# Performance work log

Hardware: AMD Instinct MI355X
Metric: run time of the kernel (lower is better)

The kernel has to match this reference:

```python
import jax, jax.numpy as jnp
import numpy as np

N, E, L, H, D_HID, D_IN, D_NEI, S_NEI, N_CLS = 30000, 480000, 2, 4, 128, 128, 64, 10, 2
HD = D_HID // H  # 32 per-head dim


def _mha(x, in_w, in_b, out_w, out_b, n_heads=4):
    # x: [N, S, D]; in_w: [D, 3D]; out_w: [D, D]
    n, s, d = x.shape
    hd = d // n_heads
    qkv = x @ in_w + in_b  # [N, S, 3D]
    q, k, v = jnp.split(qkv, 3, axis=-1)
    rs = lambda t: t.reshape(n, s, n_heads, hd).transpose(0, 2, 1, 3)  # [N,H,S,hd]
    q, k, v = rs(q), rs(k), rs(v)
    attn = jax.nn.softmax(jnp.einsum('nhqd,nhkd->nhqk', q, k) / np.sqrt(hd).astype(np.float32), axis=-1)
    o = jnp.einsum('nhqk,nhkd->nhqd', attn, v).transpose(0, 2, 1, 3).reshape(n, s, d)
    return o @ out_w + out_b


def _layer_norm(x, g, b, eps=1e-5):
    m = jnp.mean(x, axis=-1, keepdims=True)
    v = jnp.var(x, axis=-1, keepdims=True)
    return (x - m) * jax.lax.rsqrt(v + eps) * g + b


def _transformer_conv(src, dst, h, wq_i, bq_i, wk_i, bk_i, wv_i, bv_i):
    # per-head graph transformer conv: q from dst, k/v from src, edge softmax over dst
    q = (h @ wq_i + bq_i).reshape(N, H, HD)
    k = (h @ wk_i + bk_i).reshape(N, H, HD)
    v = (h @ wv_i + bv_i).reshape(N, H, HD)
    score = jnp.sum(q[dst] * k[src], axis=-1) / np.sqrt(HD).astype(np.float32)  # [E, H]
    smax = jax.ops.segment_max(score, dst, num_segments=N)  # [N, H]
    ex = jnp.exp(score - smax[dst])  # [E, H]
    denom = jax.ops.segment_sum(ex, dst, num_segments=N)  # [N, H]
    num = jax.ops.segment_sum(ex[:, :, None] * v[src], dst, num_segments=N)  # [N, H, HD]
    out = num / jnp.maximum(denom, 1e-9)[:, :, None]
    return out.reshape(N, D_HID)


def setup_inputs() -> dict:
    key = jax.random.key(0)
    ks = jax.random.split(key, 24)
    d = {}
    d['x'] = jax.random.normal(ks[0], (N, D_IN), jnp.float32)
    d['nei_features'] = jax.random.normal(ks[1], (N, S_NEI, D_NEI), jnp.float32)
    d['edge_index'] = jax.random.randint(ks[2], (L, 2, E), 0, N, jnp.int32)
    sc = 0.05
    d['w_in'] = jax.random.normal(ks[3], (D_IN, D_HID), jnp.float32) * sc
    d['b_in'] = jax.random.normal(ks[4], (D_HID,), jnp.float32) * sc
    d['mha_in_w'] = jax.random.normal(ks[5], (D_NEI, 3 * D_NEI), jnp.float32) * sc
    d['mha_in_b'] = jax.random.normal(ks[6], (3 * D_NEI,), jnp.float32) * sc
    d['mha_out_w'] = jax.random.normal(ks[7], (D_NEI, D_NEI), jnp.float32) * sc
    d['mha_out_b'] = jax.random.normal(ks[8], (D_NEI,), jnp.float32) * sc
    d['w_nei'] = jax.random.normal(ks[9], (D_NEI, D_HID), jnp.float32) * sc
    d['b_nei'] = jax.random.normal(ks[10], (D_HID,), jnp.float32) * sc
    d['wq'] = jax.random.normal(ks[11], (L, D_HID, D_HID), jnp.float32) * sc
    d['bq'] = jax.random.normal(ks[12], (L, D_HID), jnp.float32) * sc
    d['wk'] = jax.random.normal(ks[13], (L, D_HID, D_HID), jnp.float32) * sc
    d['bk'] = jax.random.normal(ks[14], (L, D_HID), jnp.float32) * sc
    d['wv'] = jax.random.normal(ks[15], (L, D_HID, D_HID), jnp.float32) * sc
    d['bv'] = jax.random.normal(ks[16], (L, D_HID), jnp.float32) * sc
    d['ln_g'] = jnp.ones((L, D_HID), jnp.float32)
    d['ln_b'] = jnp.zeros((L, D_HID), jnp.float32)
    d['w_out'] = jax.random.normal(ks[17], (D_HID, N_CLS), jnp.float32) * sc
    d['b_out'] = jnp.zeros((N_CLS,), jnp.float32)
    return d


def reference(x, nei_features, edge_index, w_in, b_in, mha_in_w, mha_in_b,
              mha_out_w, mha_out_b, w_nei, b_nei, wq, bq, wk, bk, wv, bv,
              ln_g, ln_b, w_out, b_out):
    h = x @ w_in + b_in  # input_proj
    # neighbor-feature self-attention branch (nn.MultiheadAttention, eval mode)
    nei = _mha(nei_features, mha_in_w, mha_in_b, mha_out_w, mha_out_b).mean(axis=1)
    h = h + (nei @ w_nei + b_nei)
    for i in range(L):
        src, dst = edge_index[i, 0], edge_index[i, 1]
        h = _transformer_conv(src, dst, h, wq[i], bq[i], wk[i], bk[i], wv[i], bv[i])
        h = jax.nn.relu(h)
        h = _layer_norm(h, ln_g[i], ln_b[i])
        # dropout is identity in eval mode
    return h @ w_out + b_out
```

## Files before the change

kernel.cpp:

```cpp
#include <hip/hip_runtime.h>
#include <hip/hip_bf16.h>

#define NN 30000
#define EE 480000

typedef __attribute__((ext_vector_type(8))) short short8;
typedef __attribute__((ext_vector_type(4))) short short4v;
typedef __attribute__((ext_vector_type(4))) float floatx4;
typedef unsigned short u16;

__device__ __forceinline__ u16 f2bf(float f) {
  union { float f; unsigned u; } v; v.f = f;
  unsigned u = v.u;
  u += 0x7FFFu + ((u >> 16) & 1u);
  return (u16)(u >> 16);
}
__device__ __forceinline__ float bf2f(u16 u) {
  union { unsigned u; float f; } v; v.u = ((unsigned)u) << 16;
  return v.f;
}
__device__ __forceinline__ float bflo(unsigned u) {
  union { unsigned x; float f; } v; v.x = u << 16; return v.f;
}
__device__ __forceinline__ float bfhi(unsigned u) {
  union { unsigned x; float f; } v; v.x = u & 0xFFFF0000u; return v.f;
}
__device__ __forceinline__ unsigned packbf(float a, float b) {
  return (unsigned)f2bf(a) | ((unsigned)f2bf(b) << 16);
}
__device__ __forceinline__ short8 pack8(float4 A, float4 B) {
  union { unsigned u[4]; short8 s; } r;
  r.u[0] = packbf(A.x, A.y);
  r.u[1] = packbf(A.z, A.w);
  r.u[2] = packbf(B.x, B.y);
  r.u[3] = packbf(B.z, B.w);
  return r.s;
}

#define MFMA32 __builtin_amdgcn_mfma_f32_16x16x32_bf16

#if __has_builtin(__builtin_amdgcn_mfma_f32_16x16x16bf16_1k)
__device__ __forceinline__ floatx4 MFMA16(short4v a, short4v b, floatx4 c) {
  return __builtin_amdgcn_mfma_f32_16x16x16bf16_1k(a, b, c, 0, 0, 0);
}
#else
__device__ __forceinline__ floatx4 MFMA16(short4v a, short4v b, floatx4 c) {
  asm volatile("v_mfma_f32_16x16x16_bf16 %0, %1, %2, %0"
               : "+v"(c) : "v"(a), "v"(b));
  return c;
}
#endif

__global__ __launch_bounds__(128) void k_fuse(
    const float* __restrict__ out_w, const float* __restrict__ out_b,
    const float* __restrict__ w_nei, const float* __restrict__ b_nei,
    const float* __restrict__ b_in,
    float* __restrict__ fusedW, float* __restrict__ fusedB) {
  int i = blockIdx.x, j = threadIdx.x;
  if (i < 64) {
    float a = 0.f;
    for (int kk = 0; kk < 64; ++kk) a = fmaf(out_w[i * 64 + kk], w_nei[kk * 128 + j], a);
    fusedW[i * 128 + j] = a;
  } else {
    float a = b_in[j] + b_nei[j];
    for (int kk = 0; kk < 64; ++kk) a = fmaf(out_b[kk], w_nei[kk * 128 + j], a);
    fusedB[j] = a;
  }
}

__global__ __launch_bounds__(128) void k_fuseB(
    const float* __restrict__ fusedW, const float* __restrict__ fusedB,
    const float* __restrict__ in_b, float* __restrict__ fusedB2) {
  int c = threadIdx.x;
  float a = fusedB[c];
  for (int d = 0; d < 64; ++d) a = fmaf(in_b[128 + d], fusedW[d * 128 + c], a);
  fusedB2[c] = a;
}

__global__ __launch_bounds__(128) void k_prepG(
    const float* __restrict__ in_w, const float* __restrict__ fusedW,
    float* __restrict__ G) {
  int row = blockIdx.x, c = threadIdx.x;
  int h = row >> 6, d = row & 63;
  float a = 0.f;
  for (int dd = 0; dd < 16; ++dd)
    a = fmaf(in_w[d * 192 + 128 + h * 16 + dd], fusedW[(h * 16 + dd) * 128 + c], a);
  G[row * 128 + c] = a;
}

__global__ __launch_bounds__(384) void k_prepP2(
    const float* __restrict__ w_in, const float* __restrict__ G,
    u16* __restrict__ wtP2) {
  int c = blockIdx.x, k = threadIdx.x;
  float v = (k < 128) ? w_in[(size_t)k * 128 + c] : G[(size_t)(k - 128) * 128 + c];
  wtP2[(size_t)c * 384 + k] = f2bf(v);
}

__global__ __launch_bounds__(64) void k_prepQK(
    const float* __restrict__ in_w, u16* __restrict__ wtQK) {
  int c = blockIdx.x, kk = threadIdx.x;
  float s = (c < 64) ? 0.25f : 1.f;
  wtQK[(size_t)c * 64 + kk] = f2bf(s * in_w[(size_t)kk * 192 + c]);
}

__global__ __launch_bounds__(128) void k_prepW(
    const float* __restrict__ wq, const float* __restrict__ wk,
    const float* __restrict__ wv, u16* __restrict__ wt3) {
  int bx = blockIdx.x;
  int l = bx / 384, rem = bx % 384, o = rem >> 7, c = rem & 127, k = threadIdx.x;
  const float* w = (o == 0 ? wq : (o == 1 ? wk : wv)) + (size_t)l * 16384;
  wt3[(size_t)bx * 128 + k] = f2bf(w[(size_t)k * 128 + c]);
}

__global__ __launch_bounds__(256) void k_prepX(const float* __restrict__ x, u16* __restrict__ xb) {
  int i = blockIdx.x * 256 + threadIdx.x;
  if (i < NN * 128 / 4) {
    float4 v = ((const float4*)x)[i];
    uint2 o;
    o.x = packbf(v.x, v.y);
    o.y = packbf(v.z, v.w);
    ((uint2*)xb)[i] = o;
  }
}

__global__ __launch_bounds__(640) void k_mha5(
    const float* __restrict__ xn,
    const u16* __restrict__ wtQK,
    const float* __restrict__ in_b,
    u16* __restrict__ Yb) {
  __shared__ unsigned qks[112 * 66];
  int t = threadIdx.x, w = t >> 6, l = t & 63;
  int lr = l & 15, lq = l >> 4;
  const floatx4 zf = {0.f, 0.f, 0.f, 0.f};
  size_t r0 = (size_t)blockIdx.x * 100;

  if (w < 7) {
    size_t arow = r0 + w * 16 + lr;
    if (arow > 299999) arow = 299999;
    const float* xp = xn + arow * 64 + lq * 8;
    float4 f0 = *(const float4*)xp;
    float4 f1 = *(const float4*)(xp + 4);
    float4 f2 = *(const float4*)(xp + 32);
    float4 f3 = *(const float4*)(xp + 36);
    short8 a0 = pack8(f0, f1), a1 = pack8(f2, f3);
    floatx4 acc[8];
#pragma unroll
    for (int ct = 0; ct < 8; ++ct) acc[ct] = zf;
#pragma unroll
    for (int ct = 0; ct < 8; ++ct) {
      const short8* bp = (const short8*)(wtQK + (size_t)(ct * 16 + lr) * 64);
      acc[ct] = MFMA32(a0, bp[lq], acc[ct], 0, 0, 0);
      acc[ct] = MFMA32(a1, bp[4 + lq], acc[ct], 0, 0, 0);
    }
#pragma unroll
    for (int ct = 0; ct < 4; ++ct) {
      float bq_ = in_b[ct * 16 + lr] * 0.25f;
      float bk_ = in_b[64 + ct * 16 + lr];
#pragma unroll
      for (int r = 0; r < 4; ++r)
        qks[(w * 16 + lq * 4 + r) * 66 + ct * 16 + lr] =
            packbf(acc[ct][r] + bq_, acc[ct + 4][r] + bk_);
    }
  }
  __syncthreads();

  int seqc = lr < 10 ? lr : 9;
  {
    float af0 = 0.f, af1 = 0.f, af2 = 0.f, af3 = 0.f;
#pragma unroll
    for (int h = 0; h < 4; ++h) {
      const unsigned* rp = &qks[(w * 10 + seqc) * 66 + h * 16 + lq * 4];
      uint2 u0 = *(const uint2*)rp;
      uint2 u1 = *(const uint2*)(rp + 2);
      union { unsigned u[2]; short4v s; } qv, kv;
      qv.u[0] = (u0.x & 0xFFFFu) | (u0.y << 16);
      qv.u[1] = (u1.x & 0xFFFFu) | (u1.y << 16);
      kv.u[0] = (u0.x >> 16) | (u0.y & 0xFFFF0000u);
      kv.u[1] = (u1.x >> 16) | (u1.y & 0xFFFF0000u);
      floatx4 s4 = MFMA16(kv.s, qv.s, zf);
      int j0 = lq * 4;
      float e0 = (j0 + 0 < 10) ? __expf(s4[0]) : 0.f;
      float e1 = (j0 + 1 < 10) ? __expf(s4[1]) : 0.f;
      float e2 = (j0 + 2 < 10) ? __expf(s4[2]) : 0.f;
      float e3 = (j0 + 3 < 10) ? __expf(s4[3]) : 0.f;
      float den = e0 + e1 + e2 + e3;
      den += __shfl_xor(den, 16, 64);
      den += __shfl_xor(den, 32, 64);
      float rden = 0.1f / den;
      float v0 = (lr < 10) ? e0 * rden : 0.f;
      float v1 = (lr < 10) ? e1 * rden : 0.f;
      float v2 = (lr < 10) ? e2 * rden : 0.f;
      float v3 = (lr < 10) ? e3 * rden : 0.f;
#pragma unroll
      for (int off = 1; off < 16; off <<= 1) {
        v0 += __shfl_xor(v0, off, 64);
        v1 += __shfl_xor(v1, off, 64);
        v2 += __shfl_xor(v2, off, 64);
        v3 += __shfl_xor(v3, off, 64);
      }
      if (lr == h) { af0 = v0; af1 = v1; af2 = v2; af3 = v3; }
    }
    union { unsigned u[2]; short4v s; } afv;
    afv.u[0] = packbf(af0, af1);
    afv.u[1] = packbf(af2, af3);
    size_t node = (size_t)blockIdx.x * 10 + w;
    const float* xnp = xn + node * 640;
    int jc0 = lq * 4 < 10 ? lq * 4 : 9;
    int jc1 = lq * 4 + 1 < 10 ? lq * 4 + 1 : 9;
    int jc2 = lq * 4 + 2 < 10 ? lq * 4 + 2 : 9;
    int jc3 = lq * 4 + 3 < 10 ? lq * 4 + 3 : 9;
#pragma unroll
    for (int ct = 0; ct < 4; ++ct) {
      union { unsigned u[2]; short4v s; } bx;
      bx.u[0] = packbf(xnp[jc0 * 64 + ct * 16 + lr], xnp[jc1 * 64 + ct * 16 + lr]);
      bx.u[1] = packbf(xnp[jc2 * 64 + ct * 16 + lr], xnp[jc3 * 64 + ct * 16 + lr]);
      floatx4 y4 = MFMA16(afv.s, bx.s, zf);
      if (lq == 0) {
        size_t yb = node * 256;
#pragma unroll
        for (int r = 0; r < 4; ++r)
          Yb[yb + r * 64 + ct * 16 + lr] = f2bf(y4[r]);
      }
    }
  }
}

__global__ __launch_bounds__(256) void k_proj4(
    const u16* __restrict__ xb, const u16* __restrict__ Yb,
    const u16* __restrict__ wtP2, const float* __restrict__ fusedB2,
    u16* __restrict__ hb) {
  int t = threadIdx.x, w = t >> 6, l = t & 63, lr = l & 15, lq = l >> 4;
  int row0 = blockIdx.x * 64 + w * 16;
  int arow = row0 + lr; if (arow >= NN) arow = NN - 1;
  const short8* ap = (const short8*)(xb + (size_t)arow * 128);
  const short8* yp = (const short8*)(Yb + (size_t)arow * 256);
  short8 afr[12];
#pragma unroll
  for (int kb = 0; kb < 4; ++kb) afr[kb] = ap[kb * 4 + lq];
#pragma unroll
  for (int m = 0; m < 8; ++m) afr[4 + m] = yp[m * 4 + lq];
  floatx4 acc[8];
#pragma unroll
  for (int ct = 0; ct < 8; ++ct) acc[ct] = (floatx4){0.f, 0.f, 0.f, 0.f};
#pragma unroll
  for (int ct = 0; ct < 8; ++ct) {
    const short8* bp = (const short8*)(wtP2 + (size_t)(ct * 16 + lr) * 384);
#pragma unroll
    for (int kb = 0; kb < 12; ++kb)
      acc[ct] = MFMA32(afr[kb], bp[kb * 4 + lq], acc[ct], 0, 0, 0);
  }
#pragma unroll
  for (int ct = 0; ct < 8; ++ct) {
    int col = ct * 16 + lr;
    float bias = fusedB2[col];
#pragma unroll
    for (int r = 0; r < 4; ++r) {
      int row = row0 + lq * 4 + r;
      if (row < NN) hb[(size_t)row * 128 + col] = f2bf(acc[ct][r] + bias);
    }
  }
}

__global__ __launch_bounds__(256) void k_qkv4(
    const u16* __restrict__ hb, const u16* __restrict__ wt3l,
    const float* __restrict__ bqL, const float* __restrict__ bkL,
    const float* __restrict__ bvL,
    unsigned* __restrict__ q2, unsigned* __restrict__ k2, unsigned* __restrict__ v2) {
  int t = threadIdx.x, w = t >> 6, l = t & 63, lr = l & 15, lq = l >> 4;
  int row0 = blockIdx.x * 64 + w * 16;
  int arow = row0 + lr; if (arow >= NN) arow = NN - 1;
  const short8* ap = (const short8*)(hb + (size_t)arow * 128);
  short8 a0 = ap[lq], a1 = ap[4 + lq], a2 = ap[8 + lq], a3 = ap[12 + lq];
  const short8* wt8 = (const short8*)wt3l;
  floatx4 acc[24];
#pragma unroll
  for (int ct = 0; ct < 24; ++ct) acc[ct] = (floatx4){0.f, 0.f, 0.f, 0.f};
#pragma unroll
  for (int ct = 0; ct < 24; ++ct) {
    const short8* bp = wt8 + (size_t)((ct >> 3) * 128 + (ct & 7) * 16 + lr) * 16;
    acc[ct] = MFMA32(a0, bp[lq], acc[ct], 0, 0, 0);
    acc[ct] = MFMA32(a1, bp[4 + lq], acc[ct], 0, 0, 0);
    acc[ct] = MFMA32(a2, bp[8 + lq], acc[ct], 0, 0, 0);
    acc[ct] = MFMA32(a3, bp[12 + lq], acc[ct], 0, 0, 0);
  }
#pragma unroll
  for (int o = 0; o < 3; ++o) {
    unsigned* op = o == 0 ? q2 : (o == 1 ? k2 : v2);
    const float* bp2 = o == 0 ? bqL : (o == 1 ? bkL : bvL);
#pragma unroll
    for (int cc = 0; cc < 4; ++cc) {
      int col = cc * 16 + lr;
      float blo = bp2[col], bhi = bp2[64 + col];
      floatx4 alo = acc[o * 8 + cc], ahi = acc[o * 8 + cc + 4];
#pragma unroll
      for (int r = 0; r < 4; ++r) {
        int row = row0 + lq * 4 + r;
        if (row < NN)
          op[(size_t)row * 64 + col] = packbf(alo[r] + blo, ahi[r] + bhi);
      }
    }
  }
}

__global__ __launch_bounds__(256) void k_fill(const int* __restrict__ ei,
                                              int* __restrict__ cnt,
                                              int* __restrict__ esrc) {
  int gthr = blockIdx.x * 256 + threadIdx.x;
  if (gthr < 2 * EE) {
    int l = gthr >= EE;
    int e = gthr - l * EE;
    int s = ei[(size_t)(2 * l) * EE + e];
    int d = ei[(size_t)(2 * l + 1) * EE + e];
    int c = atomicAdd(&cnt[l * NN + d], 1);
    if (c < 64) esrc[((size_t)l * NN + d) * 64 + c] = s;
  }
}

__global__ __launch_bounds__(256) void k_sagg5(
    const unsigned* __restrict__ q2, const unsigned* __restrict__ k2,
    const unsigned* __restrict__ v2, const int* __restrict__ esrc,
    const int* __restrict__ cnt, const float* __restrict__ g,
    const float* __restrict__ bb, u16* __restrict__ hb,
    const float* __restrict__ wo, const float* __restrict__ bo,
    float* __restrict__ outp) {
  int t = threadIdx.x, w = t >> 6, l = t & 63;
  int e = l >> 4, dd = l & 15;
  int n = blockIdx.x * 4 + w;
  int deg = cnt[n]; if (deg > 64) deg = 64;
  const int* sp = esrc + (size_t)n * 64;
  uint4 qp = *(const uint4*)(q2 + (size_t)n * 64 + dd * 4);
  float ql0 = bflo(qp.x), ql1 = bflo(qp.y), ql2 = bflo(qp.z), ql3 = bflo(qp.w);
  float qh0 = bfhi(qp.x), qh1 = bfhi(qp.y), qh2 = bfhi(qp.z), qh3 = bfhi(qp.w);
  float d0 = 0.f, d1 = 0.f;
  float al0 = 0.f, al1 = 0.f, al2 = 0.f, al3 = 0.f;
  float ah0 = 0.f, ah1 = 0.f, ah2 = 0.f, ah3 = 0.f;
  uint4 kp_c, vp_c;
  bool v_c = false;
  if (deg > 0) {
    int ii = (e < deg) ? e : deg - 1;
    v_c = e < deg;
    int s = sp[ii];
    kp_c = *(const uint4*)(k2 + (size_t)s * 64 + dd * 4);
    vp_c = *(const uint4*)(v2 + (size_t)s * 64 + dd * 4);
  }
  for (int base = 0; base < deg; base += 4) {
    uint4 kp_n, vp_n;
    bool v_n = false;
    int nb = base + 4;
    if (nb < deg) {
      int idx = nb + e;
      int ii = (idx < deg) ? idx : deg - 1;
      v_n = idx < deg;
      int s = sp[ii];
      kp_n = *(const uint4*)(k2 + (size_t)s * 64 + dd * 4);
      vp_n = *(const uint4*)(v2 + (size_t)s * 64 + dd * 4);
    }
    float r0 = ql0 * bflo(kp_c.x) + ql1 * bflo(kp_c.y) + ql2 * bflo(kp_c.z) + ql3 * bflo(kp_c.w);
    float r1 = qh0 * bfhi(kp_c.x) + qh1 * bfhi(kp_c.y) + qh2 * bfhi(kp_c.z) + qh3 * bfhi(kp_c.w);
    r0 += __shfl_xor(r0, 1, 64); r0 += __shfl_xor(r0, 2, 64); r0 += __shfl_xor(r0, 4, 64);
    r1 += __shfl_xor(r1, 1, 64); r1 += __shfl_xor(r1, 2, 64); r1 += __shfl_xor(r1, 4, 64);
    float p0 = v_c ? __expf(r0 * 0.17677669529663687f) : 0.f;
    float p1 = v_c ? __expf(r1 * 0.17677669529663687f) : 0.f;
    d0 += p0; d1 += p1;
    al0 = fmaf(p0, bflo(vp_c.x), al0); al1 = fmaf(p0, bflo(vp_c.y), al1);
    al2 = fmaf(p0, bflo(vp_c.z), al2); al3 = fmaf(p0, bflo(vp_c.w), al3);
    ah0 = fmaf(p1, bfhi(vp_c.x), ah0); ah1 = fmaf(p1, bfhi(vp_c.y), ah1);
    ah2 = fmaf(p1, bfhi(vp_c.z), ah2); ah3 = fmaf(p1, bfhi(vp_c.w), ah3);
    kp_c = kp_n; vp_c = vp_n; v_c = v_n;
  }
  d0 += __shfl_xor(d0, 16, 64); d0 += __shfl_xor(d0, 32, 64);
  d1 += __shfl_xor(d1, 16, 64); d1 += __shfl_xor(d1, 32, 64);
  al0 += __shfl_xor(al0, 16, 64); al0 += __shfl_xor(al0, 32, 64);
  al1 += __shfl_xor(al1, 16, 64); al1 += __shfl_xor(al1, 32, 64);
  al2 += __shfl_xor(al2, 16, 64); al2 += __shfl_xor(al2, 32, 64);
  al3 += __shfl_xor(al3, 16, 64); al3 += __shfl_xor(al3, 32, 64);
  ah0 += __shfl_xor(ah0, 16, 64); ah0 += __shfl_xor(ah0, 32, 64);
  ah1 += __shfl_xor(ah1, 16, 64); ah1 += __shfl_xor(ah1, 32, 64);
  ah2 += __shfl_xor(ah2, 16, 64); ah2 += __shfl_xor(ah2, 32, 64);
  ah3 += __shfl_xor(ah3, 16, 64); ah3 += __shfl_xor(ah3, 32, 64);
  float rd0 = 1.f / fmaxf(d0, 1e-9f), rd1 = 1.f / fmaxf(d1, 1e-9f);
  float ol0 = fmaxf(al0 * rd0, 0.f), ol1 = fmaxf(al1 * rd0, 0.f);
  float ol2 = fmaxf(al2 * rd0, 0.f), ol3 = fmaxf(al3 * rd0, 0.f);
  float oh0 = fmaxf(ah0 * rd1, 0.f), oh1 = fmaxf(ah1 * rd1, 0.f);
  float oh2 = fmaxf(ah2 * rd1, 0.f), oh3 = fmaxf(ah3 * rd1, 0.f);
  float s1 = ol0 + ol1 + ol2 + ol3 + oh0 + oh1 + oh2 + oh3;
  float s2 = ol0 * ol0 + ol1 * ol1 + ol2 * ol2 + ol3 * ol3 +
             oh0 * oh0 + oh1 * oh1 + oh2 * oh2 + oh3 * oh3;
  s1 += __shfl_xor(s1, 1, 64); s1 += __shfl_xor(s1, 2, 64);
  s1 += __shfl_xor(s1, 4, 64); s1 += __shfl_xor(s1, 8, 64);
  s2 += __shfl_xor(s2, 1, 64); s2 += __shfl_xor(s2, 2, 64);
  s2 += __shfl_xor(s2, 4, 64); s2 += __shfl_xor(s2, 8, 64);
  float mean = s1 * (1.f / 128.f);
  float var = s2 * (1.f / 128.f) - mean * mean;
  float rs = rsqrtf(var + 1e-5f);
  if (e == 0) {
    floatx4 gl = *(const floatx4*)(g + dd * 4);
    floatx4 bl = *(const floatx4*)(bb + dd * 4);
    floatx4 gh = *(const floatx4*)(g + 64 + dd * 4);
    floatx4 bh = *(const floatx4*)(bb + 64 + dd * 4);
    float hl0 = (ol0 - mean) * rs * gl[0] + bl[0];
    float hl1 = (ol1 - mean) * rs * gl[1] + bl[1];
    float hl2 = (ol2 - mean) * rs * gl[2] + bl[2];
    float hl3 = (ol3 - mean) * rs * gl[3] + bl[3];
    float hh0 = (oh0 - mean) * rs * gh[0] + bh[0];
    float hh1 = (oh1 - mean) * rs * gh[1] + bh[1];
    float hh2 = (oh2 - mean) * rs * gh[2] + bh[2];
    float hh3 = (oh3 - mean) * rs * gh[3] + bh[3];
    if (outp == nullptr) {
      uint2 w0, w1;
      w0.x = packbf(hl0, hl1); w0.y = packbf(hl2, hl3);
      w1.x = packbf(hh0, hh1); w1.y = packbf(hh2, hh3);
      *(uint2*)(hb + (size_t)n * 128 + dd * 4) = w0;
      *(uint2*)(hb + (size_t)n * 128 + 64 + dd * 4) = w1;
    } else {
      const float2* wo2 = (const float2*)wo;
      float2 wa0 = wo2[dd * 4], wa1 = wo2[dd * 4 + 1];
      float2 wa2 = wo2[dd * 4 + 2], wa3 = wo2[dd * 4 + 3];
      float2 wb0 = wo2[64 + dd * 4], wb1 = wo2[64 + dd * 4 + 1];
      float2 wb2 = wo2[64 + dd * 4 + 2], wb3 = wo2[64 + dd * 4 + 3];
      float p0 = hl0 * wa0.x + hl1 * wa1.x + hl2 * wa2.x + hl3 * wa3.x +
                 hh0 * wb0.x + hh1 * wb1.x + hh2 * wb2.x + hh3 * wb3.x;
      float p1 = hl0 * wa0.y + hl1 * wa1.y + hl2 * wa2.y + hl3 * wa3.y +
                 hh0 * wb0.y + hh1 * wb1.y + hh2 * wb2.y + hh3 * wb3.y;
      p0 += __shfl_xor(p0, 1, 16); p0 += __shfl_xor(p0, 2, 16);
      p0 += __shfl_xor(p0, 4, 16); p0 += __shfl_xor(p0, 8, 16);
      p1 += __shfl_xor(p1, 1, 16); p1 += __shfl_xor(p1, 2, 16);
      p1 += __shfl_xor(p1, 4, 16); p1 += __shfl_xor(p1, 8, 16);
      if (dd == 0) {
        outp[n * 2] = p0 + bo[0];
        outp[n * 2 + 1] = p1 + bo[1];
      }
    }
  }
}

extern "C" void kernel_launch(void* const* d_in, const int* in_sizes, int n_in,
                              void* d_out, int out_size, void* d_ws, size_t ws_size,
                              hipStream_t stream) {
  const float* x = (const float*)d_in[0];
  const float* neif = (const float*)d_in[1];
  const int* ei = (const int*)d_in[2];
  const float* w_in = (const float*)d_in[3];
  const float* b_in = (const float*)d_in[4];
  const float* mha_in_w = (const float*)d_in[5];
  const float* mha_in_b = (const float*)d_in[6];
  const float* mha_out_w = (const float*)d_in[7];
  const float* mha_out_b = (const float*)d_in[8];
  const float* w_nei = (const float*)d_in[9];
  const float* b_nei = (const float*)d_in[10];
  const float* wq = (const float*)d_in[11];
  const float* bq = (const float*)d_in[12];
  const float* wk = (const float*)d_in[13];
  const float* bk = (const float*)d_in[14];
  const float* wv = (const float*)d_in[15];
  const float* bv = (const float*)d_in[16];
  const float* ln_g = (const float*)d_in[17];
  const float* ln_b = (const float*)d_in[18];
  const float* w_out = (const float*)d_in[19];
  const float* b_out = (const float*)d_in[20];
  float* out = (float*)d_out;

  char* wsb = (char*)d_ws;
  size_t off = 0;
  unsigned* q2 = (unsigned*)(wsb + off); off += (size_t)NN * 64 * 4;
  unsigned* k2 = (unsigned*)(wsb + off); off += (size_t)NN * 64 * 4;
  unsigned* v2 = (unsigned*)(wsb + off); off += (size_t)NN * 64 * 4;
  int* esrc = (int*)(wsb + off);         off += (size_t)2 * NN * 64 * 4;
  u16* Yb = (u16*)(wsb + off);           off += (size_t)NN * 256 * 2;
  u16* hb = (u16*)(wsb + off);           off += (size_t)NN * 128 * 2;
  u16* xb = (u16*)(wsb + off);           off += (size_t)NN * 128 * 2;
  u16* wt3 = (u16*)(wsb + off);          off += (size_t)768 * 128 * 2;
  u16* wtP2 = (u16*)(wsb + off);         off += (size_t)128 * 384 * 2;
  u16* wtQK = (u16*)(wsb + off);         off += (size_t)128 * 64 * 2;
  float* G = (float*)(wsb + off);        off += (size_t)256 * 128 * 4;
  float* fusedW = (float*)(wsb + off);   off += 64 * 128 * 4;
  float* fusedB = (float*)(wsb + off);   off += 128 * 4;
  float* fusedB2 = (float*)(wsb + off);  off += 128 * 4;
  int* cnt = (int*)(wsb + off);          off += (size_t)2 * NN * 4;

  k_fuse<<<65, 128, 0, stream>>>(mha_out_w, mha_out_b, w_nei, b_nei, b_in, fusedW, fusedB);
  k_fuseB<<<1, 128, 0, stream>>>(fusedW, fusedB, mha_in_b, fusedB2);
  k_prepG<<<256, 128, 0, stream>>>(mha_in_w, fusedW, G);
  k_prepP2<<<128, 384, 0, stream>>>(w_in, G, wtP2);
  k_prepQK<<<128, 64, 0, stream>>>(mha_in_w, wtQK);
  k_prepW<<<768, 128, 0, stream>>>(wq, wk, wv, wt3);
  k_prepX<<<3750, 256, 0, stream>>>(x, xb);

  k_mha5<<<3000, 640, 0, stream>>>(neif, wtQK, mha_in_b, Yb);
  k_proj4<<<469, 256, 0, stream>>>(xb, Yb, wtP2, fusedB2, hb);

  hipMemsetAsync(cnt, 0, 2 * NN * sizeof(int), stream);
  k_fill<<<3750, 256, 0, stream>>>(ei, cnt, esrc);

  for (int l = 0; l < 2; ++l) {
    k_qkv4<<<469, 256, 0, stream>>>(hb, wt3 + (size_t)l * 3 * 128 * 128,
                                    bq + l * 128, bk + l * 128, bv + l * 128,
                                    q2, k2, v2);
    k_sagg5<<<NN / 4, 256, 0, stream>>>(q2, k2, v2, esrc + (size_t)l * NN * 64,
                                        cnt + l * NN, ln_g + l * 128,
                                        ln_b + l * 128, hb,
                                        w_out, b_out, l == 0 ? nullptr : out);
  }
}
```

Measured before the change: 337.9 us.

## Merge prep kernels, stage neighbor features in LDS, dual-stream edge aggregation

Several small weight-prep kernels are merged into fewer launches, and the separate bf16 conversion of x is removed so the projection kernel reads fp32 x and packs it itself. The MHA kernel keeps a transposed bf16 copy of the neighbor features in shared memory, so the second MFMA reads them from LDS instead of reloading scattered fp32 values from global memory. The aggregation kernel now processes eight edges per iteration using two independent accumulator sets, adding memory-level parallelism. The cost is more registers and LDS, which may lower occupancy.

```diff
diff --git a/kernel.cpp b/kernel.cpp
--- a/kernel.cpp
+++ b/kernel.cpp
@@ -68,24 +68,22 @@
   }
 }
 
-__global__ __launch_bounds__(128) void k_fuseB(
-    const float* __restrict__ fusedW, const float* __restrict__ fusedB,
-    const float* __restrict__ in_b, float* __restrict__ fusedB2) {
-  int c = threadIdx.x;
-  float a = fusedB[c];
-  for (int d = 0; d < 64; ++d) a = fmaf(in_b[128 + d], fusedW[d * 128 + c], a);
-  fusedB2[c] = a;
-}
-
-__global__ __launch_bounds__(128) void k_prepG(
+__global__ __launch_bounds__(128) void k_prepB(
     const float* __restrict__ in_w, const float* __restrict__ fusedW,
-    float* __restrict__ G) {
-  int row = blockIdx.x, c = threadIdx.x;
-  int h = row >> 6, d = row & 63;
-  float a = 0.f;
-  for (int dd = 0; dd < 16; ++dd)
-    a = fmaf(in_w[d * 192 + 128 + h * 16 + dd], fusedW[(h * 16 + dd) * 128 + c], a);
-  G[row * 128 + c] = a;
+    const float* __restrict__ fusedB, const float* __restrict__ in_b,
+    float* __restrict__ G, float* __restrict__ fusedB2) {
+  int bx = blockIdx.x, c = threadIdx.x;
+  if (bx < 256) {
+    int h = bx >> 6, d = bx & 63;
+    float a = 0.f;
+    for (int dd = 0; dd < 16; ++dd)
+      a = fmaf(in_w[d * 192 + 128 + h * 16 + dd], fusedW[(h * 16 + dd) * 128 + c], a);
+    G[bx * 128 + c] = a;
+  } else {
+    float a = fusedB[c];
+    for (int d = 0; d < 64; ++d) a = fmaf(in_b[128 + d], fusedW[d * 128 + c], a);
+    fusedB2[c] = a;
+  }
 }
 
 __global__ __launch_bounds__(384) void k_prepP2(
@@ -96,46 +94,43 @@
   wtP2[(size_t)c * 384 + k] = f2bf(v);
 }
 
-__global__ __launch_bounds__(64) void k_prepQK(
-    const float* __restrict__ in_w, u16* __restrict__ wtQK) {
-  int c = blockIdx.x, kk = threadIdx.x;
-  float s = (c < 64) ? 0.25f : 1.f;
-  wtQK[(size_t)c * 64 + kk] = f2bf(s * in_w[(size_t)kk * 192 + c]);
-}
-
-__global__ __launch_bounds__(128) void k_prepW(
+__global__ __launch_bounds__(128) void k_prepA(
     const float* __restrict__ wq, const float* __restrict__ wk,
-    const float* __restrict__ wv, u16* __restrict__ wt3) {
-  int bx = blockIdx.x;
-  int l = bx / 384, rem = bx % 384, o = rem >> 7, c = rem & 127, k = threadIdx.x;
-  const float* w = (o == 0 ? wq : (o == 1 ? wk : wv)) + (size_t)l * 16384;
-  wt3[(size_t)bx * 128 + k] = f2bf(w[(size_t)k * 128 + c]);
-}
-
-__global__ __launch_bounds__(256) void k_prepX(const float* __restrict__ x, u16* __restrict__ xb) {
-  int i = blockIdx.x * 256 + threadIdx.x;
-  if (i < NN * 128 / 4) {
-    float4 v = ((const float4*)x)[i];
-    uint2 o;
-    o.x = packbf(v.x, v.y);
-    o.y = packbf(v.z, v.w);
-    ((uint2*)xb)[i] = o;
-  }
-}
-
-__global__ __launch_bounds__(640) void k_mha5(
+    const float* __restrict__ wv, const float* __restrict__ in_w,
+    u16* __restrict__ wt3, u16* __restrict__ wtQK) {
+  int bx = blockIdx.x, t = threadIdx.x;
+  if (bx < 768) {
+    int l = bx / 384, rem = bx % 384, o = rem >> 7, c = rem & 127;
+    const float* w = (o == 0 ? wq : (o == 1 ? wk : wv)) + (size_t)l * 16384;
+    wt3[(size_t)bx * 128 + t] = f2bf(w[(size_t)t * 128 + c]);
+  } else {
+    int c = (bx - 768) * 2 + (t >> 6), kk = t & 63;
+    float s = (c < 64) ? 0.25f : 1.f;
+    wtQK[(size_t)c * 64 + kk] = f2bf(s * in_w[(size_t)kk * 192 + c]);
+  }
+}
+
+__global__ __launch_bounds__(640) void k_mha6b(
     const float* __restrict__ xn,
     const u16* __restrict__ wtQK,
     const float* __restrict__ in_b,
     u16* __restrict__ Yb) {
   __shared__ unsigned qks[112 * 66];
+  __shared__ u16 xsT[64 * 160];
   int t = threadIdx.x, w = t >> 6, l = t & 63;
   int lr = l & 15, lq = l >> 4;
   const floatx4 zf = {0.f, 0.f, 0.f, 0.f};
   size_t r0 = (size_t)blockIdx.x * 100;
 
+  {
+    int d = t / 10, nd = t - d * 10;
+#pragma unroll
+    for (int j = 10; j < 16; ++j) xsT[d * 160 + nd * 16 + j] = 0;
+  }
+
   if (w < 7) {
-    size_t arow = r0 + w * 16 + lr;
+    int row = w * 16 + lr;
+    size_t arow = r0 + row;
     if (arow > 299999) arow = 299999;
     const float* xp = xn + arow * 64 + lq * 8;
     float4 f0 = *(const float4*)xp;
@@ -143,6 +138,17 @@
     float4 f2 = *(const float4*)(xp + 32);
     float4 f3 = *(const float4*)(xp + 36);
     short8 a0 = pack8(f0, f1), a1 = pack8(f2, f3);
+    if (row < 100) {
+      int node = row / 10, j = row - node * 10;
+      int base = node * 16 + j;
+      union { short8 s; u16 u[8]; } ua0, ua1;
+      ua0.s = a0; ua1.s = a1;
+#pragma unroll
+      for (int i = 0; i < 8; ++i) {
+        xsT[(lq * 8 + i) * 160 + base] = ua0.u[i];
+        xsT[(32 + lq * 8 + i) * 160 + base] = ua1.u[i];
+      }
+    }
     floatx4 acc[8];
 #pragma unroll
     for (int ct = 0; ct < 8; ++ct) acc[ct] = zf;
@@ -204,17 +210,10 @@
     afv.u[0] = packbf(af0, af1);
     afv.u[1] = packbf(af2, af3);
     size_t node = (size_t)blockIdx.x * 10 + w;
-    const float* xnp = xn + node * 640;
-    int jc0 = lq * 4 < 10 ? lq * 4 : 9;
-    int jc1 = lq * 4 + 1 < 10 ? lq * 4 + 1 : 9;
-    int jc2 = lq * 4 + 2 < 10 ? lq * 4 + 2 : 9;
-    int jc3 = lq * 4 + 3 < 10 ? lq * 4 + 3 : 9;
 #pragma unroll
     for (int ct = 0; ct < 4; ++ct) {
-      union { unsigned u[2]; short4v s; } bx;
-      bx.u[0] = packbf(xnp[jc0 * 64 + ct * 16 + lr], xnp[jc1 * 64 + ct * 16 + lr]);
-      bx.u[1] = packbf(xnp[jc2 * 64 + ct * 16 + lr], xnp[jc3 * 64 + ct * 16 + lr]);
-      floatx4 y4 = MFMA16(afv.s, bx.s, zf);
+      short4v bx = *(const short4v*)&xsT[(ct * 16 + lr) * 160 + w * 16 + lq * 4];
+      floatx4 y4 = MFMA16(afv.s, bx, zf);
       if (lq == 0) {
         size_t yb = node * 256;
 #pragma unroll
@@ -225,18 +224,22 @@
   }
 }
 
-__global__ __launch_bounds__(256) void k_proj4(
-    const u16* __restrict__ xb, const u16* __restrict__ Yb,
+__global__ __launch_bounds__(256) void k_proj5(
+    const float* __restrict__ x, const u16* __restrict__ Yb,
     const u16* __restrict__ wtP2, const float* __restrict__ fusedB2,
     u16* __restrict__ hb) {
   int t = threadIdx.x, w = t >> 6, l = t & 63, lr = l & 15, lq = l >> 4;
   int row0 = blockIdx.x * 64 + w * 16;
   int arow = row0 + lr; if (arow >= NN) arow = NN - 1;
-  const short8* ap = (const short8*)(xb + (size_t)arow * 128);
+  const float* xp = x + (size_t)arow * 128;
   const short8* yp = (const short8*)(Yb + (size_t)arow * 256);
   short8 afr[12];
 #pragma unroll
-  for (int kb = 0; kb < 4; ++kb) afr[kb] = ap[kb * 4 + lq];
+  for (int kb = 0; kb < 4; ++kb) {
+    float4 fa = *(const float4*)(xp + kb * 32 + lq * 8);
+    float4 fb = *(const float4*)(xp + kb * 32 + lq * 8 + 4);
+    afr[kb] = pack8(fa, fb);
+  }
 #pragma unroll
   for (int m = 0; m < 8; ++m) afr[4 + m] = yp[m * 4 + lq];
   floatx4 acc[8];
@@ -316,13 +319,14 @@
   }
 }
 
-__global__ __launch_bounds__(256) void k_sagg5(
+__global__ __launch_bounds__(256) void k_sagg6(
     const unsigned* __restrict__ q2, const unsigned* __restrict__ k2,
     const unsigned* __restrict__ v2, const int* __restrict__ esrc,
     const int* __restrict__ cnt, const float* __restrict__ g,
     const float* __restrict__ bb, u16* __restrict__ hb,
     const float* __restrict__ wo, const float* __restrict__ bo,
     float* __restrict__ outp) {
+  const float SC = 0.17677669529663687f;
   int t = threadIdx.x, w = t >> 6, l = t & 63;
   int e = l >> 4, dd = l & 15;
   int n = blockIdx.x * 4 + w;
@@ -331,43 +335,66 @@
   uint4 qp = *(const uint4*)(q2 + (size_t)n * 64 + dd * 4);
   float ql0 = bflo(qp.x), ql1 = bflo(qp.y), ql2 = bflo(qp.z), ql3 = bflo(qp.w);
   float qh0 = bfhi(qp.x), qh1 = bfhi(qp.y), qh2 = bfhi(qp.z), qh3 = bfhi(qp.w);
-  float d0 = 0.f, d1 = 0.f;
-  float al0 = 0.f, al1 = 0.f, al2 = 0.f, al3 = 0.f;
-  float ah0 = 0.f, ah1 = 0.f, ah2 = 0.f, ah3 = 0.f;
-  uint4 kp_c, vp_c;
-  bool v_c = false;
+  float dA0 = 0.f, dA1 = 0.f, dB0 = 0.f, dB1 = 0.f;
+  float alA0 = 0.f, alA1 = 0.f, alA2 = 0.f, alA3 = 0.f;
+  float ahA0 = 0.f, ahA1 = 0.f, ahA2 = 0.f, ahA3 = 0.f;
+  float alB0 = 0.f, alB1 = 0.f, alB2 = 0.f, alB3 = 0.f;
+  float ahB0 = 0.f, ahB1 = 0.f, ahB2 = 0.f, ahB3 = 0.f;
+  uint4 kA = {0, 0, 0, 0}, vA = {0, 0, 0, 0};
+  uint4 kB = {0, 0, 0, 0}, vB = {0, 0, 0, 0};
+  bool mA = false, mB = false;
   if (deg > 0) {
-    int ii = (e < deg) ? e : deg - 1;
-    v_c = e < deg;
-    int s = sp[ii];
-    kp_c = *(const uint4*)(k2 + (size_t)s * 64 + dd * 4);
-    vp_c = *(const uint4*)(v2 + (size_t)s * 64 + dd * 4);
-  }
-  for (int base = 0; base < deg; base += 4) {
-    uint4 kp_n, vp_n;
-    bool v_n = false;
-    int nb = base + 4;
+    int iA = e < deg ? e : deg - 1;           mA = e < deg;
+    int iB = 4 + e < deg ? 4 + e : deg - 1;   mB = 4 + e < deg;
+    int sA = sp[iA], sB = sp[iB];
+    kA = *(const uint4*)(k2 + (size_t)sA * 64 + dd * 4);
+    vA = *(const uint4*)(v2 + (size_t)sA * 64 + dd * 4);
+    kB = *(const uint4*)(k2 + (size_t)sB * 64 + dd * 4);
+    vB = *(const uint4*)(v2 + (size_t)sB * 64 + dd * 4);
+  }
+  for (int base = 0; base < deg; base += 8) {
+    uint4 kAn = {0, 0, 0, 0}, vAn = {0, 0, 0, 0};
+    uint4 kBn = {0, 0, 0, 0}, vBn = {0, 0, 0, 0};
+    bool mAn = false, mBn = false;
+    int nb = base + 8;
     if (nb < deg) {
-      int idx = nb + e;
-      int ii = (idx < deg) ? idx : deg - 1;
-      v_n = idx < deg;
-      int s = sp[ii];
-      kp_n = *(const uint4*)(k2 + (size_t)s * 64 + dd * 4);
-      vp_n = *(const uint4*)(v2 + (size_t)s * 64 + dd * 4);
-    }
-    float r0 = ql0 * bflo(kp_c.x) + ql1 * bflo(kp_c.y) + ql2 * bflo(kp_c.z) + ql3 * bflo(kp_c.w);
-    float r1 = qh0 * bfhi(kp_c.x) + qh1 * bfhi(kp_c.y) + qh2 * bfhi(kp_c.z) + qh3 * bfhi(kp_c.w);
-    r0 += __shfl_xor(r0, 1, 64); r0 += __shfl_xor(r0, 2, 64); r0 += __shfl_xor(r0, 4, 64);
-    r1 += __shfl_xor(r1, 1, 64); r1 += __shfl_xor(r1, 2, 64); r1 += __shfl_xor(r1, 4, 64);
-    float p0 = v_c ? __expf(r0 * 0.17677669529663687f) : 0.f;
-    float p1 = v_c ? __expf(r1 * 0.17677669529663687f) : 0.f;
-    d0 += p0; d1 += p1;
-    al0 = fmaf(p0, bflo(vp_c.x), al0); al1 = fmaf(p0, bflo(vp_c.y), al1);
-    al2 = fmaf(p0, bflo(vp_c.z), al2); al3 = fmaf(p0, bflo(vp_c.w), al3);
-    ah0 = fmaf(p1, bfhi(vp_c.x), ah0); ah1 = fmaf(p1, bfhi(vp_c.y), ah1);
-    ah2 = fmaf(p1, bfhi(vp_c.z), ah2); ah3 = fmaf(p1, bfhi(vp_c.w), ah3);
-    kp_c = kp_n; vp_c = vp_n; v_c = v_n;
-  }
+      int iA = nb + e < deg ? nb + e : deg - 1;         mAn = nb + e < deg;
+      int iB = nb + 4 + e < deg ? nb + 4 + e : deg - 1; mBn = nb + 4 + e < deg;
+      int sA = sp[iA], sB = sp[iB];
+      kAn = *(const uint4*)(k2 + (size_t)sA * 64 + dd * 4);
+      vAn = *(const uint4*)(v2 + (size_t)sA * 64 + dd * 4);
+      kBn = *(const uint4*)(k2 + (size_t)sB * 64 + dd * 4);
+      vBn = *(const uint4*)(v2 + (size_t)sB * 64 + dd * 4);
+    }
+    float rA0 = ql0 * bflo(kA.x) + ql1 * bflo(kA.y) + ql2 * bflo(kA.z) + ql3 * bflo(kA.w);
+    float rA1 = qh0 * bfhi(kA.x) + qh1 * bfhi(kA.y) + qh2 * bfhi(kA.z) + qh3 * bfhi(kA.w);
+    float rB0 = ql0 * bflo(kB.x) + ql1 * bflo(kB.y) + ql2 * bflo(kB.z) + ql3 * bflo(kB.w);
+    float rB1 = qh0 * bfhi(kB.x) + qh1 * bfhi(kB.y) + qh2 * bfhi(kB.z) + qh3 * bfhi(kB.w);
+    rA0 += __shfl_xor(rA0, 1, 64); rB0 += __shfl_xor(rB0, 1, 64);
+    rA1 += __shfl_xor(rA1, 1, 64); rB1 += __shfl_xor(rB1, 1, 64);
+    rA0 += __shfl_xor(rA0, 2, 64); rB0 += __shfl_xor(rB0, 2, 64);
+    rA1 += __shfl_xor(rA1, 2, 64); rB1 += __shfl_xor(rB1, 2, 64);
+    rA0 += __shfl_xor(rA0, 4, 64); rB0 += __shfl_xor(rB0, 4, 64);
+    rA1 += __shfl_xor(rA1, 4, 64); rB1 += __shfl_xor(rB1, 4, 64);
+    float pA0 = mA ? __expf(rA0 * SC) : 0.f;
+    float pA1 = mA ? __expf(rA1 * SC) : 0.f;
+    float pB0 = mB ? __expf(rB0 * SC) : 0.f;
+    float pB1 = mB ? __expf(rB1 * SC) : 0.f;
+    dA0 += pA0; dA1 += pA1; dB0 += pB0; dB1 += pB1;
+    alA0 = fmaf(pA0, bflo(vA.x), alA0); alA1 = fmaf(pA0, bflo(vA.y), alA1);
+    alA2 = fmaf(pA0, bflo(vA.z), alA2); alA3 = fmaf(pA0, bflo(vA.w), alA3);
+    ahA0 = fmaf(pA1, bfhi(vA.x), ahA0); ahA1 = fmaf(pA1, bfhi(vA.y), ahA1);
+    ahA2 = fmaf(pA1, bfhi(vA.z), ahA2); ahA3 = fmaf(pA1, bfhi(vA.w), ahA3);
+    alB0 = fmaf(pB0, bflo(vB.x), alB0); alB1 = fmaf(pB0, bflo(vB.y), alB1);
+    alB2 = fmaf(pB0, bflo(vB.z), alB2); alB3 = fmaf(pB0, bflo(vB.w), alB3);
+    ahB0 = fmaf(pB1, bfhi(vB.x), ahB0); ahB1 = fmaf(pB1, bfhi(vB.y), ahB1);
+    ahB2 = fmaf(pB1, bfhi(vB.z), ahB2); ahB3 = fmaf(pB1, bfhi(vB.w), ahB3);
+    kA = kAn; vA = vAn; mA = mAn;
+    kB = kBn; vB = vBn; mB = mBn;
+  }
+  float d0 = dA0 + dB0, d1 = dA1 + dB1;
+  float al0 = alA0 + alB0, al1 = alA1 + alB1, al2 = alA2 + alB2, al3 = alA3 + alB3;
+  float ah0 = ahA0 + ahB0, ah1 = ahA1 + ahB1, ah2 = ahA2 + ahB2, ah3 = ahA3 + ahB3;
   d0 += __shfl_xor(d0, 16, 64); d0 += __shfl_xor(d0, 32, 64);
   d1 += __shfl_xor(d1, 16, 64); d1 += __shfl_xor(d1, 32, 64);
   al0 += __shfl_xor(al0, 16, 64); al0 += __shfl_xor(al0, 32, 64);
@@ -468,7 +495,6 @@
   int* esrc = (int*)(wsb + off);         off += (size_t)2 * NN * 64 * 4;
   u16* Yb = (u16*)(wsb + off);           off += (size_t)NN * 256 * 2;
   u16* hb = (u16*)(wsb + off);           off += (size_t)NN * 128 * 2;
-  u16* xb = (u16*)(wsb + off);           off += (size_t)NN * 128 * 2;
   u16* wt3 = (u16*)(wsb + off);          off += (size_t)768 * 128 * 2;
   u16* wtP2 = (u16*)(wsb + off);         off += (size_t)128 * 384 * 2;
   u16* wtQK = (u16*)(wsb + off);         off += (size_t)128 * 64 * 2;
@@ -479,15 +505,12 @@
   int* cnt = (int*)(wsb + off);          off += (size_t)2 * NN * 4;
 
   k_fuse<<<65, 128, 0, stream>>>(mha_out_w, mha_out_b, w_nei, b_nei, b_in, fusedW, fusedB);
-  k_fuseB<<<1, 128, 0, stream>>>(fusedW, fusedB, mha_in_b, fusedB2);
-  k_prepG<<<256, 128, 0, stream>>>(mha_in_w, fusedW, G);
+  k_prepB<<<257, 128, 0, stream>>>(mha_in_w, fusedW, fusedB, mha_in_b, G, fusedB2);
   k_prepP2<<<128, 384, 0, stream>>>(w_in, G, wtP2);
-  k_prepQK<<<128, 64, 0, stream>>>(mha_in_w, wtQK);
-  k_prepW<<<768, 128, 0, stream>>>(wq, wk, wv, wt3);
-  k_prepX<<<3750, 256, 0, stream>>>(x, xb);
-
-  k_mha5<<<3000, 640, 0, stream>>>(neif, wtQK, mha_in_b, Yb);
-  k_proj4<<<469, 256, 0, stream>>>(xb, Yb, wtP2, fusedB2, hb);
+  k_prepA<<<832, 128, 0, stream>>>(wq, wk, wv, mha_in_w, wt3, wtQK);
+
+  k_mha6b<<<3000, 640, 0, stream>>>(neif, wtQK, mha_in_b, Yb);
+  k_proj5<<<469, 256, 0, stream>>>(x, Yb, wtP2, fusedB2, hb);
 
   hipMemsetAsync(cnt, 0, 2 * NN * sizeof(int), stream);
   k_fill<<<3750, 256, 0, stream>>>(ei, cnt, esrc);
@@ -496,7 +519,7 @@
     k_qkv4<<<469, 256, 0, stream>>>(hb, wt3 + (size_t)l * 3 * 128 * 128,
                                     bq + l * 128, bk + l * 128, bv + l * 128,
                                     q2, k2, v2);
-    k_sagg5<<<NN / 4, 256, 0, stream>>>(q2, k2, v2, esrc + (size_t)l * NN * 64,
+    k_sagg6<<<NN / 4, 256, 0, stream>>>(q2, k2, v2, esrc + (size_t)l * NN * 64,
                                         cnt + l * NN, ln_g + l * 128,
                                         ln_b + l * 128, hb,
                                         w_out, b_out, l == 0 ? nullptr : out);
```

Measured after the change: 324.0 us. -4.1%, faster.
